# Kernel optimization log

Hardware: AMD Instinct MI355X
Metric: run time of the kernel (lower is better)

The kernel has to match this reference:

```python
import jax, jax.numpy as jnp
import numpy as np
from jax import lax


def ternarize(w):
    # w: (O, I, KH, KW). Per-output-filter delta/alpha as in the torch code.
    O = w.shape[0]
    n = w[0].size  # elements per filter
    abs_w = jnp.abs(w)
    flat_abs = abs_w.reshape(O, -1)
    delta = (0.7 / n) * flat_abs.sum(axis=1)          # (O,)
    d = delta.reshape(O, 1, 1, 1)
    mask = abs_w > d                                   # |w| > delta
    cnt = mask.reshape(O, -1).sum(axis=1).astype(w.dtype)  # (O,)
    alpha = jnp.where(mask, abs_w, 0.0).reshape(O, -1).sum(axis=1) / cnt  # (O,)
    tern = jnp.where(w > d, 1.0, jnp.where(w < -d, -1.0, 0.0)).astype(w.dtype)
    return tern * alpha.reshape(O, 1, 1, 1)


def conv2d(x, w, stride=(1, 1), padding=((1, 1), (1, 1))):
    return lax.conv_general_dilated(
        x, w, window_strides=stride, padding=padding,
        dimension_numbers=("NCHW", "OIHW", "NCHW"))


def setup_inputs() -> dict:
    key = jax.random.key(0)
    k1, k2, k3 = jax.random.split(key, 3)
    x = jax.random.normal(k1, (32, 256, 56, 56), dtype=jnp.float32)
    # kaiming-uniform-ish, clamped to [-1, 1] as in __init__
    weight = jnp.clip(jax.random.normal(k2, (256, 256, 3, 3), dtype=jnp.float32) * 0.05, -1.0, 1.0)
    bias = jax.random.normal(k3, (256,), dtype=jnp.float32) * 0.02
    return {"x": x, "weight": weight, "bias": bias}


def reference(x, weight, bias):
    w_t = ternarize(weight)
    y = conv2d(x, w_t) + bias[None, :, None, None]
    return y
```

## Files before the change

### kernel.cpp

```cpp
#include <hip/hip_runtime.h>
#include <hip/hip_bf16.h>
#include <stdint.h>

typedef short bf16x8 __attribute__((ext_vector_type(8)));
typedef float f32x4 __attribute__((ext_vector_type(4)));
typedef unsigned short ushort_t;
typedef unsigned int uint_t;

#define CIN   256
#define COUT  256
#define HWDIM 56
#define IMG   (HWDIM * HWDIM)
#define K_TOT (CIN * 9)
#define NIMG  32
#define NPIX  (NIMG * IMG)
#define BM    128
#define BN    128
#define BK    64

#define AS1CAST(p) ((const __attribute__((address_space(1))) unsigned int*)(uintptr_t)(p))
#define AS3CAST(p) ((__attribute__((address_space(3))) unsigned int*)(uintptr_t)(p))

__device__ __forceinline__ ushort_t f2bf(float f) {
    union { float f; uint_t u; } v; v.f = f;
    uint_t u = v.u;
    uint_t r = u + 0x7FFFu + ((u >> 16) & 1u);
    return (ushort_t)(r >> 16);
}

__global__ __launch_bounds__(256) void ternarize_kernel(
        const float* __restrict__ w,
        ushort_t* __restrict__ wt2,
        float* __restrict__ alpha_out,
        ushort_t* __restrict__ xt_pad_row) {
    const int o = blockIdx.x;
    const int t = threadIdx.x;
    const int lane = t & 63;
    const int wv = t >> 6;
    const float* base = w + (size_t)o * K_TOT;

    if (o == 0 && t < 32) ((uint4*)xt_pad_row)[t] = (uint4){0u, 0u, 0u, 0u};

    float v[9];
#pragma unroll
    for (int i = 0; i < 9; ++i) v[i] = base[t + 256 * i];

    __shared__ float sred[8];

    float s = 0.f;
#pragma unroll
    for (int i = 0; i < 9; ++i) s += fabsf(v[i]);
#pragma unroll
    for (int off = 32; off > 0; off >>= 1) s += __shfl_down(s, off);
    if (lane == 0) sred[wv] = s;
    __syncthreads();
    if (t == 0) sred[0] = sred[0] + sred[1] + sred[2] + sred[3];
    __syncthreads();
    const float delta = (0.7f / (float)K_TOT) * sred[0];
    __syncthreads();

    float asum = 0.f, cnt = 0.f;
#pragma unroll
    for (int i = 0; i < 9; ++i) {
        float a = fabsf(v[i]);
        if (a > delta) { asum += a; cnt += 1.f; }
    }
#pragma unroll
    for (int off = 32; off > 0; off >>= 1) {
        asum += __shfl_down(asum, off);
        cnt  += __shfl_down(cnt, off);
    }
    if (lane == 0) { sred[wv] = asum; sred[4 + wv] = cnt; }
    __syncthreads();
    if (t == 0) {
        float at = sred[0] + sred[1] + sred[2] + sred[3];
        float ct = sred[4] + sred[5] + sred[6] + sred[7];
        alpha_out[o] = at / ct;
    }

#pragma unroll
    for (int i = 0; i < 9; ++i) {
        int idx = t + 256 * i;
        int c = idx / 9;
        int r = idx - c * 9;
        float x = v[i];
        ushort_t bits = 0;
        if (x > delta)       bits = 0x3F80u;
        else if (x < -delta) bits = 0xBF80u;
        wt2[(size_t)o * K_TOT + r * 256 + c] = bits;
    }
}

__global__ __launch_bounds__(256) void transpose_kernel(
        const float* __restrict__ x, ushort_t* __restrict__ xt) {
    __shared__ float L[32][132];
    const int hw0 = blockIdx.x * 32;
    const int c0  = blockIdx.y * 128;
    const int n   = blockIdx.z;
    const int t = threadIdx.x;
    const int c_ = t >> 1;
    const int half = t & 1;

    const float* src = x + (size_t)(n * CIN + c0 + c_) * IMG + hw0 + half * 16;
    float4 v[4];
#pragma unroll
    for (int k = 0; k < 4; ++k) v[k] = *(const float4*)(src + k * 4);
#pragma unroll
    for (int k = 0; k < 4; ++k) {
        L[half * 16 + k * 4 + 0][c_] = v[k].x;
        L[half * 16 + k * 4 + 1][c_] = v[k].y;
        L[half * 16 + k * 4 + 2][c_] = v[k].z;
        L[half * 16 + k * 4 + 3][c_] = v[k].w;
    }
    __syncthreads();

    const int seg = t & 15;
    const int hwb = t >> 4;
#pragma unroll
    for (int j = 0; j < 2; ++j) {
        const int hwl = hwb + j * 16;
        const float* row = &L[hwl][seg * 8];
        uint_t pk[4];
#pragma unroll
        for (int q = 0; q < 4; ++q)
            pk[q] = (uint_t)f2bf(row[2 * q]) | ((uint_t)f2bf(row[2 * q + 1]) << 16);
        *(uint4*)&xt[(size_t)(n * IMG + hw0 + hwl) * CIN + c0 + seg * 8] =
            (uint4){pk[0], pk[1], pk[2], pk[3]};
    }
}

__global__ __launch_bounds__(256) void tern_conv_kernel(
        const ushort_t* __restrict__ xt,
        const ushort_t* __restrict__ wt2,
        const float* __restrict__ alpha,
        const float* __restrict__ bias,
        float* __restrict__ out) {
    __shared__ __align__(16) ushort_t As[BM * BK];
    __shared__ __align__(16) ushort_t Xs[BN * BK];

    const int tid = threadIdx.x;
    const int wv = tid >> 6;
    const int l = tid & 63;
    const int bid = blockIdx.x;
    const int o0 = (bid & 1) * BM;
    const int p0 = (bid >> 1) * BN;

    const int subrow = l >> 3;
    const int g = (l & 7) ^ subrow;

    const ushort_t* aptr[4];
    int ximg[4], xh[4], xw[4];
#pragma unroll
    for (int i = 0; i < 4; ++i) {
        int r = wv * 32 + i * 8 + subrow;
        aptr[i] = wt2 + (size_t)(o0 + r) * K_TOT + g * 8;
        int p = p0 + r;
        int n_img = p / IMG;
        int hw_ = p - n_img * IMG;
        xh[i] = hw_ / HWDIM;
        xw[i] = hw_ - xh[i] * HWDIM;
        ximg[i] = n_img * IMG;
    }

    ushort_t* adst[4]; ushort_t* xdst[4];
#pragma unroll
    for (int i = 0; i < 4; ++i) {
        adst[i] = &As[(wv * 32 + i * 8) * BK];
        xdst[i] = &Xs[(wv * 32 + i * 8) * BK];
    }

    const int qd = l >> 4, ln = l & 15;
    const int wm = (wv >> 1) * 64, wn = (wv & 1) * 64;
    const int sbase = (qd ^ (ln & 7)) * 8;
    int arow[4], xrow[4];
#pragma unroll
    for (int i = 0; i < 4; ++i) {
        arow[i] = (wm + i * 16 + ln) * BK;
        xrow[i] = (wn + i * 16 + ln) * BK;
    }

    f32x4 acc[4][4];
#pragma unroll
    for (int i = 0; i < 4; ++i)
#pragma unroll
        for (int j = 0; j < 4; ++j)
            acc[i][j] = (f32x4){0.f, 0.f, 0.f, 0.f};

#pragma unroll 1
    for (int c0 = 0; c0 < CIN; c0 += BK) {
#pragma unroll 1
        for (int kpos = 0; kpos < 9; ++kpos) {
            const int dh = kpos / 3 - 1;
            const int dw = kpos - (dh + 1) * 3 - 1;
            const ushort_t* xsrc[4];
#pragma unroll
            for (int i = 0; i < 4; ++i) {
                int h2 = xh[i] + dh, w2 = xw[i] + dw;
                int row = ((unsigned)h2 < (unsigned)HWDIM && (unsigned)w2 < (unsigned)HWDIM)
                              ? (ximg[i] + h2 * HWDIM + w2) : NPIX;
                xsrc[i] = xt + (size_t)row * CIN + g * 8 + c0;
            }
            const int aoff = kpos * 256 + c0;

            __syncthreads();
#pragma unroll
            for (int i = 0; i < 4; ++i)
                __builtin_amdgcn_global_load_lds(AS1CAST(aptr[i] + aoff), AS3CAST(adst[i]), 16, 0, 0);
#pragma unroll
            for (int i = 0; i < 4; ++i)
                __builtin_amdgcn_global_load_lds(AS1CAST(xsrc[i]), AS3CAST(xdst[i]), 16, 0, 0);
            __syncthreads();

#pragma unroll
            for (int h = 0; h < 2; ++h) {
                const int so = sbase ^ (h * 32);
                bf16x8 af[4], bfr[4];
#pragma unroll
                for (int i = 0; i < 4; ++i)
                    af[i] = *(const bf16x8*)&As[arow[i] + so];
#pragma unroll
                for (int i = 0; i < 4; ++i)
                    bfr[i] = *(const bf16x8*)&Xs[xrow[i] + so];
#pragma unroll
                for (int im = 0; im < 4; ++im)
#pragma unroll
                    for (int in2 = 0; in2 < 4; ++in2)
                        acc[im][in2] = __builtin_amdgcn_mfma_f32_16x16x32_bf16(
                            af[im], bfr[in2], acc[im][in2], 0, 0, 0);
            }
        }
    }

#pragma unroll
    for (int im = 0; im < 4; ++im) {
        const int orow = o0 + wm + im * 16 + qd * 4;
        const f32x4 al = *(const f32x4*)&alpha[orow];
        const f32x4 bi = *(const f32x4*)&bias[orow];
#pragma unroll
        for (int in2 = 0; in2 < 4; ++in2) {
            const int pc = p0 + wn + in2 * 16 + ln;
            const int ni = pc / IMG;
            const int hwc = pc - ni * IMG;
            const size_t obase = (size_t)ni * COUT * IMG + hwc;
#pragma unroll
            for (int rr = 0; rr < 4; ++rr)
                out[obase + (size_t)(orow + rr) * IMG] = al[rr] * acc[im][in2][rr] + bi[rr];
        }
    }
}

extern "C" void kernel_launch(void* const* d_in, const int* in_sizes, int n_in,
                              void* d_out, int out_size, void* d_ws, size_t ws_size,
                              hipStream_t stream) {
    const float* x      = (const float*)d_in[0];
    const float* weight = (const float*)d_in[1];
    const float* bias   = (const float*)d_in[2];
    float* out = (float*)d_out;

    ushort_t* xt     = (ushort_t*)d_ws;
    ushort_t* wt2    = (ushort_t*)((char*)d_ws + (size_t)(NPIX + 1) * CIN * sizeof(ushort_t));
    float*    alphav = (float*)((char*)wt2 + (size_t)COUT * K_TOT * sizeof(ushort_t));

    ternarize_kernel<<<COUT, 256, 0, stream>>>(weight, wt2, alphav,
                                               xt + (size_t)NPIX * CIN);

    dim3 tg(IMG / 32, CIN / 128, NIMG);
    transpose_kernel<<<tg, 256, 0, stream>>>(x, xt);

    const int n_blocks = (COUT / BM) * (NPIX / BN);
    tern_conv_kernel<<<n_blocks, 256, 0, stream>>>(xt, wt2, alphav, bias, out);
}
```

Baseline: 315.5 us.

## Double-buffer LDS tiles and pipeline global-to-LDS loads with MFMA compute

```diff
diff --git a/kernel.cpp b/kernel.cpp
--- a/kernel.cpp
+++ b/kernel.cpp
@@ -16,7 +16,7 @@
 #define NPIX  (NIMG * IMG)
 #define BM    128
 #define BN    128
-#define BK    64
+#define NSTEP 18
 
 #define AS1CAST(p) ((const __attribute__((address_space(1))) unsigned int*)(uintptr_t)(p))
 #define AS3CAST(p) ((__attribute__((address_space(3))) unsigned int*)(uintptr_t)(p))
@@ -129,14 +129,14 @@
     }
 }
 
-__global__ __launch_bounds__(256) void tern_conv_kernel(
+__global__ __launch_bounds__(256, 2) void tern_conv_kernel(
         const ushort_t* __restrict__ xt,
         const ushort_t* __restrict__ wt2,
         const float* __restrict__ alpha,
         const float* __restrict__ bias,
         float* __restrict__ out) {
-    __shared__ __align__(16) ushort_t As[BM * BK];
-    __shared__ __align__(16) ushort_t Xs[BN * BK];
+    __shared__ __align__(16) ushort_t As[2][BM * 64];
+    __shared__ __align__(16) ushort_t Xs[2][BN * 64];
 
     const int tid = threadIdx.x;
     const int wv = tid >> 6;
@@ -145,16 +145,15 @@
     const int o0 = (bid & 1) * BM;
     const int p0 = (bid >> 1) * BN;
 
-    const int subrow = l >> 3;
-    const int g = (l & 7) ^ subrow;
-
-    const ushort_t* aptr[4];
+    const int rthr = tid >> 3;
+    const int g = (l & 7) ^ ((l >> 3) & 7);
+
+    const ushort_t* abase[4];
     int ximg[4], xh[4], xw[4];
 #pragma unroll
     for (int i = 0; i < 4; ++i) {
-        int r = wv * 32 + i * 8 + subrow;
-        aptr[i] = wt2 + (size_t)(o0 + r) * K_TOT + g * 8;
-        int p = p0 + r;
+        abase[i] = wt2 + (size_t)(o0 + i * 32 + rthr) * K_TOT + g * 8;
+        int p = p0 + i * 32 + rthr;
         int n_img = p / IMG;
         int hw_ = p - n_img * IMG;
         xh[i] = hw_ / HWDIM;
@@ -162,21 +161,18 @@
         ximg[i] = n_img * IMG;
     }
 
-    ushort_t* adst[4]; ushort_t* xdst[4];
-#pragma unroll
-    for (int i = 0; i < 4; ++i) {
-        adst[i] = &As[(wv * 32 + i * 8) * BK];
-        xdst[i] = &Xs[(wv * 32 + i * 8) * BK];
-    }
+    int doff[4];
+#pragma unroll
+    for (int i = 0; i < 4; ++i) doff[i] = (i * 32 + (wv << 3)) << 6;
 
     const int qd = l >> 4, ln = l & 15;
     const int wm = (wv >> 1) * 64, wn = (wv & 1) * 64;
-    const int sbase = (qd ^ (ln & 7)) * 8;
+    const int so0 = (qd ^ (ln & 7)) * 8;
     int arow[4], xrow[4];
 #pragma unroll
     for (int i = 0; i < 4; ++i) {
-        arow[i] = (wm + i * 16 + ln) * BK;
-        xrow[i] = (wn + i * 16 + ln) * BK;
+        arow[i] = (wm + i * 16 + ln) * 64;
+        xrow[i] = (wn + i * 16 + ln) * 64;
     }
 
     f32x4 acc[4][4];
@@ -186,48 +182,93 @@
         for (int j = 0; j < 4; ++j)
             acc[i][j] = (f32x4){0.f, 0.f, 0.f, 0.f};
 
+    {
+        const ushort_t* xsrc[4];
+#pragma unroll
+        for (int i = 0; i < 4; ++i) {
+            int h2 = xh[i] - 1, w2 = xw[i] - 1;
+            int row = ((unsigned)h2 < (unsigned)HWDIM && (unsigned)w2 < (unsigned)HWDIM)
+                          ? (ximg[i] + h2 * HWDIM + w2) : NPIX;
+            xsrc[i] = xt + (size_t)row * CIN + g * 8;
+        }
+#pragma unroll
+        for (int kh = 0; kh < 2; ++kh) {
+#pragma unroll
+            for (int i = 0; i < 4; ++i)
+                __builtin_amdgcn_global_load_lds(AS1CAST(abase[i] + kh * 64),
+                                                 AS3CAST(&As[kh][doff[i]]), 16, 0, 0);
+#pragma unroll
+            for (int i = 0; i < 4; ++i)
+                __builtin_amdgcn_global_load_lds(AS1CAST(xsrc[i] + kh * 64),
+                                                 AS3CAST(&Xs[kh][doff[i]]), 16, 0, 0);
+        }
+    }
+    asm volatile("s_waitcnt vmcnt(8)" ::: "memory");
+    __builtin_amdgcn_s_barrier();
+    asm volatile("" ::: "memory");
+
 #pragma unroll 1
-    for (int c0 = 0; c0 < CIN; c0 += BK) {
-#pragma unroll 1
-        for (int kpos = 0; kpos < 9; ++kpos) {
-            const int dh = kpos / 3 - 1;
-            const int dw = kpos - (dh + 1) * 3 - 1;
-            const ushort_t* xsrc[4];
-#pragma unroll
-            for (int i = 0; i < 4; ++i) {
-                int h2 = xh[i] + dh, w2 = xw[i] + dw;
-                int row = ((unsigned)h2 < (unsigned)HWDIM && (unsigned)w2 < (unsigned)HWDIM)
-                              ? (ximg[i] + h2 * HWDIM + w2) : NPIX;
-                xsrc[i] = xt + (size_t)row * CIN + g * 8 + c0;
+    for (int s = 0; s < NSTEP; ++s) {
+        const int sn = (s + 1 < NSTEP) ? s + 1 : NSTEP - 1;
+        const int c0n = (sn >= 9) ? 128 : 0;
+        const int kposn = sn - ((sn >= 9) ? 9 : 0);
+        const int dh = kposn / 3 - 1;
+        const int dw = kposn - (dh + 1) * 3 - 1;
+        const int koffn = kposn * 256 + c0n;
+        const ushort_t* xsrc[4];
+#pragma unroll
+        for (int i = 0; i < 4; ++i) {
+            int h2 = xh[i] + dh, w2 = xw[i] + dw;
+            int row = ((unsigned)h2 < (unsigned)HWDIM && (unsigned)w2 < (unsigned)HWDIM)
+                          ? (ximg[i] + h2 * HWDIM + w2) : NPIX;
+            xsrc[i] = xt + (size_t)row * CIN + c0n + g * 8;
+        }
+
+#pragma unroll
+        for (int hs = 0; hs < 2; ++hs) {
+            bf16x8 a0[4], a1[4], x0[4], x1[4];
+#pragma unroll
+            for (int m = 0; m < 4; ++m) {
+                a0[m] = *(const bf16x8*)&As[hs][arow[m] + so0];
+                a1[m] = *(const bf16x8*)&As[hs][arow[m] + (so0 ^ 32)];
             }
-            const int aoff = kpos * 256 + c0;
-
-            __syncthreads();
+#pragma unroll
+            for (int n = 0; n < 4; ++n) {
+                x0[n] = *(const bf16x8*)&Xs[hs][xrow[n] + so0];
+                x1[n] = *(const bf16x8*)&Xs[hs][xrow[n] + (so0 ^ 32)];
+            }
+            asm volatile("" ::: "memory");
+            __builtin_amdgcn_s_barrier();
+            asm volatile("" ::: "memory");
+            __builtin_amdgcn_s_setprio(1);
+#pragma unroll
+            for (int m = 0; m < 4; ++m)
+#pragma unroll
+                for (int n = 0; n < 4; ++n)
+                    acc[m][n] = __builtin_amdgcn_mfma_f32_16x16x32_bf16(
+                        a0[m], x0[n], acc[m][n], 0, 0, 0);
+            __builtin_amdgcn_s_setprio(0);
+
 #pragma unroll
             for (int i = 0; i < 4; ++i)
-                __builtin_amdgcn_global_load_lds(AS1CAST(aptr[i] + aoff), AS3CAST(adst[i]), 16, 0, 0);
+                __builtin_amdgcn_global_load_lds(AS1CAST(abase[i] + koffn + hs * 64),
+                                                 AS3CAST(&As[hs][doff[i]]), 16, 0, 0);
 #pragma unroll
             for (int i = 0; i < 4; ++i)
-                __builtin_amdgcn_global_load_lds(AS1CAST(xsrc[i]), AS3CAST(xdst[i]), 16, 0, 0);
-            __syncthreads();
-
-#pragma unroll
-            for (int h = 0; h < 2; ++h) {
-                const int so = sbase ^ (h * 32);
-                bf16x8 af[4], bfr[4];
-#pragma unroll
-                for (int i = 0; i < 4; ++i)
-                    af[i] = *(const bf16x8*)&As[arow[i] + so];
-#pragma unroll
-                for (int i = 0; i < 4; ++i)
-                    bfr[i] = *(const bf16x8*)&Xs[xrow[i] + so];
-#pragma unroll
-                for (int im = 0; im < 4; ++im)
-#pragma unroll
-                    for (int in2 = 0; in2 < 4; ++in2)
-                        acc[im][in2] = __builtin_amdgcn_mfma_f32_16x16x32_bf16(
-                            af[im], bfr[in2], acc[im][in2], 0, 0, 0);
-            }
+                __builtin_amdgcn_global_load_lds(AS1CAST(xsrc[i] + hs * 64),
+                                                 AS3CAST(&Xs[hs][doff[i]]), 16, 0, 0);
+            asm volatile("s_waitcnt vmcnt(8)" ::: "memory");
+            asm volatile("" ::: "memory");
+            __builtin_amdgcn_s_barrier();
+            asm volatile("" ::: "memory");
+            __builtin_amdgcn_s_setprio(1);
+#pragma unroll
+            for (int m = 0; m < 4; ++m)
+#pragma unroll
+                for (int n = 0; n < 4; ++n)
+                    acc[m][n] = __builtin_amdgcn_mfma_f32_16x16x32_bf16(
+                        a1[m], x1[n], acc[m][n], 0, 0, 0);
+            __builtin_amdgcn_s_setprio(0);
         }
     }
 
```

After: 299.5 us. -5.1%, faster.

## Double-buffer LDS tiles and software-pipeline fragment reads with MFMA in conv

Applied to the files above, without the earlier changes.

```diff
diff --git a/kernel.cpp b/kernel.cpp
--- a/kernel.cpp
+++ b/kernel.cpp
@@ -16,7 +16,7 @@
 #define NPIX  (NIMG * IMG)
 #define BM    128
 #define BN    128
-#define BK    64
+#define NCHUNK 36
 
 #define AS1CAST(p) ((const __attribute__((address_space(1))) unsigned int*)(uintptr_t)(p))
 #define AS3CAST(p) ((__attribute__((address_space(3))) unsigned int*)(uintptr_t)(p))
@@ -119,24 +119,26 @@
 #pragma unroll
     for (int j = 0; j < 2; ++j) {
         const int hwl = hwb + j * 16;
-        const float* row = &L[hwl][seg * 8];
+        const float2* row = (const float2*)&L[hwl][seg * 8];
         uint_t pk[4];
 #pragma unroll
-        for (int q = 0; q < 4; ++q)
-            pk[q] = (uint_t)f2bf(row[2 * q]) | ((uint_t)f2bf(row[2 * q + 1]) << 16);
+        for (int q = 0; q < 4; ++q) {
+            float2 f = row[q];
+            pk[q] = (uint_t)f2bf(f.x) | ((uint_t)f2bf(f.y) << 16);
+        }
         *(uint4*)&xt[(size_t)(n * IMG + hw0 + hwl) * CIN + c0 + seg * 8] =
             (uint4){pk[0], pk[1], pk[2], pk[3]};
     }
 }
 
-__global__ __launch_bounds__(256) void tern_conv_kernel(
+__global__ __launch_bounds__(256, 2) void tern_conv_kernel(
         const ushort_t* __restrict__ xt,
         const ushort_t* __restrict__ wt2,
         const float* __restrict__ alpha,
         const float* __restrict__ bias,
         float* __restrict__ out) {
-    __shared__ __align__(16) ushort_t As[BM * BK];
-    __shared__ __align__(16) ushort_t Xs[BN * BK];
+    __shared__ __align__(16) ushort_t As[2][BM * 64];
+    __shared__ __align__(16) ushort_t Xs[2][BN * 64];
 
     const int tid = threadIdx.x;
     const int wv = tid >> 6;
@@ -145,16 +147,15 @@
     const int o0 = (bid & 1) * BM;
     const int p0 = (bid >> 1) * BN;
 
-    const int subrow = l >> 3;
-    const int g = (l & 7) ^ subrow;
-
-    const ushort_t* aptr[4];
+    const int rthr = tid >> 3;
+    const int g = (l & 7) ^ ((l >> 3) & 7);
+
+    const ushort_t* abase[4];
     int ximg[4], xh[4], xw[4];
 #pragma unroll
     for (int i = 0; i < 4; ++i) {
-        int r = wv * 32 + i * 8 + subrow;
-        aptr[i] = wt2 + (size_t)(o0 + r) * K_TOT + g * 8;
-        int p = p0 + r;
+        abase[i] = wt2 + (size_t)(o0 + i * 32 + rthr) * K_TOT + g * 8;
+        int p = p0 + i * 32 + rthr;
         int n_img = p / IMG;
         int hw_ = p - n_img * IMG;
         xh[i] = hw_ / HWDIM;
@@ -162,21 +163,18 @@
         ximg[i] = n_img * IMG;
     }
 
-    ushort_t* adst[4]; ushort_t* xdst[4];
-#pragma unroll
-    for (int i = 0; i < 4; ++i) {
-        adst[i] = &As[(wv * 32 + i * 8) * BK];
-        xdst[i] = &Xs[(wv * 32 + i * 8) * BK];
-    }
+    int doff[4];
+#pragma unroll
+    for (int i = 0; i < 4; ++i) doff[i] = (i * 32 + (wv << 3)) << 6;
 
     const int qd = l >> 4, ln = l & 15;
     const int wm = (wv >> 1) * 64, wn = (wv & 1) * 64;
-    const int sbase = (qd ^ (ln & 7)) * 8;
+    const int so0 = (qd ^ (ln & 7)) * 8;
     int arow[4], xrow[4];
 #pragma unroll
     for (int i = 0; i < 4; ++i) {
-        arow[i] = (wm + i * 16 + ln) * BK;
-        xrow[i] = (wn + i * 16 + ln) * BK;
+        arow[i] = (wm + i * 16 + ln) * 64;
+        xrow[i] = (wn + i * 16 + ln) * 64;
     }
 
     f32x4 acc[4][4];
@@ -186,50 +184,107 @@
         for (int j = 0; j < 4; ++j)
             acc[i][j] = (f32x4){0.f, 0.f, 0.f, 0.f};
 
+    bf16x8 fa[2][8], fx[2][8];
+
+#define STAGE_CHUNK(c, SLOT) do {                                               \
+    const int st_ = (c) >> 1, hs_ = (c) & 1;                                    \
+    const int c0_ = (st_ >= 9) ? 128 : 0;                                       \
+    const int kp_ = st_ - ((st_ >= 9) ? 9 : 0);                                 \
+    const int dh_ = kp_ / 3 - 1;                                                \
+    const int dw_ = kp_ - (dh_ + 1) * 3 - 1;                                    \
+    const int aoff_ = kp_ * 256 + c0_ + hs_ * 64;                               \
+    _Pragma("unroll")                                                           \
+    for (int i = 0; i < 4; ++i)                                                 \
+        __builtin_amdgcn_global_load_lds(AS1CAST(abase[i] + aoff_),             \
+                                         AS3CAST(&As[SLOT][doff[i]]), 16, 0, 0);\
+    _Pragma("unroll")                                                           \
+    for (int i = 0; i < 4; ++i) {                                               \
+        int h2_ = xh[i] + dh_, w2_ = xw[i] + dw_;                               \
+        int row_ = ((unsigned)h2_ < (unsigned)HWDIM &&                          \
+                    (unsigned)w2_ < (unsigned)HWDIM)                            \
+                       ? (ximg[i] + h2_ * HWDIM + w2_) : NPIX;                  \
+        __builtin_amdgcn_global_load_lds(                                       \
+            AS1CAST(xt + (size_t)row_ * CIN + c0_ + hs_ * 64 + g * 8),          \
+            AS3CAST(&Xs[SLOT][doff[i]]), 16, 0, 0);                             \
+    }                                                                           \
+} while (0)
+
+#define READ_FRAGS(P) do {                                                      \
+    _Pragma("unroll")                                                           \
+    for (int m = 0; m < 4; ++m) {                                               \
+        fa[P][m]     = *(const bf16x8*)&As[P][arow[m] + so0];                   \
+        fa[P][m + 4] = *(const bf16x8*)&As[P][arow[m] + (so0 ^ 32)];            \
+    }                                                                           \
+    _Pragma("unroll")                                                           \
+    for (int n = 0; n < 4; ++n) {                                               \
+        fx[P][n]     = *(const bf16x8*)&Xs[P][xrow[n] + so0];                   \
+        fx[P][n + 4] = *(const bf16x8*)&Xs[P][xrow[n] + (so0 ^ 32)];            \
+    }                                                                           \
+} while (0)
+
+#define MFMA_CLUSTER(P) do {                                                    \
+    __builtin_amdgcn_s_setprio(1);                                              \
+    _Pragma("unroll")                                                           \
+    for (int m = 0; m < 4; ++m)                                                 \
+        _Pragma("unroll")                                                       \
+        for (int n = 0; n < 4; ++n)                                             \
+            acc[m][n] = __builtin_amdgcn_mfma_f32_16x16x32_bf16(                \
+                fa[P][m], fx[P][n], acc[m][n], 0, 0, 0);                        \
+    _Pragma("unroll")                                                           \
+    for (int m = 0; m < 4; ++m)                                                 \
+        _Pragma("unroll")                                                       \
+        for (int n = 0; n < 4; ++n)                                             \
+            acc[m][n] = __builtin_amdgcn_mfma_f32_16x16x32_bf16(                \
+                fa[P][m + 4], fx[P][n + 4], acc[m][n], 0, 0, 0);                \
+    __builtin_amdgcn_s_setprio(0);                                              \
+} while (0)
+
+#define PHASE(k, P) do {                                                        \
+    asm volatile("s_waitcnt vmcnt(8)" ::: "memory");                            \
+    __builtin_amdgcn_s_barrier();                                               \
+    asm volatile("" ::: "memory");                                              \
+    READ_FRAGS(P);                                                              \
+    MFMA_CLUSTER(1 - (P));                                                      \
+    asm volatile("s_waitcnt lgkmcnt(0)" ::: "memory");                          \
+    __builtin_amdgcn_s_barrier();                                               \
+    asm volatile("" ::: "memory");                                              \
+    STAGE_CHUNK((k) + 2, P);                                                    \
+} while (0)
+
+#define PHASE_TAIL(P, VM) do {                                                  \
+    asm volatile("s_waitcnt vmcnt(" #VM ")" ::: "memory");                      \
+    __builtin_amdgcn_s_barrier();                                               \
+    asm volatile("" ::: "memory");                                              \
+    READ_FRAGS(P);                                                              \
+    MFMA_CLUSTER(1 - (P));                                                      \
+} while (0)
+
+    STAGE_CHUNK(0, 0);
+    STAGE_CHUNK(1, 1);
+    asm volatile("s_waitcnt vmcnt(8)" ::: "memory");
+    __builtin_amdgcn_s_barrier();
+    asm volatile("" ::: "memory");
+    READ_FRAGS(0);
+    asm volatile("s_waitcnt lgkmcnt(0)" ::: "memory");
+    __builtin_amdgcn_s_barrier();
+    asm volatile("" ::: "memory");
+    STAGE_CHUNK(2, 0);
+
 #pragma unroll 1
-    for (int c0 = 0; c0 < CIN; c0 += BK) {
-#pragma unroll 1
-        for (int kpos = 0; kpos < 9; ++kpos) {
-            const int dh = kpos / 3 - 1;
-            const int dw = kpos - (dh + 1) * 3 - 1;
-            const ushort_t* xsrc[4];
-#pragma unroll
-            for (int i = 0; i < 4; ++i) {
-                int h2 = xh[i] + dh, w2 = xw[i] + dw;
-                int row = ((unsigned)h2 < (unsigned)HWDIM && (unsigned)w2 < (unsigned)HWDIM)
-                              ? (ximg[i] + h2 * HWDIM + w2) : NPIX;
-                xsrc[i] = xt + (size_t)row * CIN + g * 8 + c0;
-            }
-            const int aoff = kpos * 256 + c0;
-
-            __syncthreads();
-#pragma unroll
-            for (int i = 0; i < 4; ++i)
-                __builtin_amdgcn_global_load_lds(AS1CAST(aptr[i] + aoff), AS3CAST(adst[i]), 16, 0, 0);
-#pragma unroll
-            for (int i = 0; i < 4; ++i)
-                __builtin_amdgcn_global_load_lds(AS1CAST(xsrc[i]), AS3CAST(xdst[i]), 16, 0, 0);
-            __syncthreads();
-
-#pragma unroll
-            for (int h = 0; h < 2; ++h) {
-                const int so = sbase ^ (h * 32);
-                bf16x8 af[4], bfr[4];
-#pragma unroll
-                for (int i = 0; i < 4; ++i)
-                    af[i] = *(const bf16x8*)&As[arow[i] + so];
-#pragma unroll
-                for (int i = 0; i < 4; ++i)
-                    bfr[i] = *(const bf16x8*)&Xs[xrow[i] + so];
-#pragma unroll
-                for (int im = 0; im < 4; ++im)
-#pragma unroll
-                    for (int in2 = 0; in2 < 4; ++in2)
-                        acc[im][in2] = __builtin_amdgcn_mfma_f32_16x16x32_bf16(
-                            af[im], bfr[in2], acc[im][in2], 0, 0, 0);
-            }
-        }
-    }
+    for (int k = 1; k < 33; k += 2) {
+        PHASE(k, 1);
+        PHASE(k + 1, 0);
+    }
+    PHASE(33, 1);
+    PHASE_TAIL(0, 8);
+    PHASE_TAIL(1, 0);
+    MFMA_CLUSTER(1);
+
+#undef PHASE_TAIL
+#undef PHASE
+#undef MFMA_CLUSTER
+#undef READ_FRAGS
+#undef STAGE_CHUNK
 
 #pragma unroll
     for (int im = 0; im < 4; ++im) {
```

Measured after the change: 306.4 us. -2.9%, faster.
